# Kernel tuning notes

Measured on AMD Instinct MI355X. Metric: run time of the kernel, lower is better.

Reference implementation:

```python
import jax, jax.numpy as jnp
import numpy as np

L = 512       # seq_len (capped by hard-coded max_length=512)
LEN = 2048    # input feature dim ('length')
D = 2048      # d_model
H = 16        # num_heads
DH = D // H   # d_head = 128
FF = 8192     # FFN hidden
EPS = 1e-5


def _pos_encoding(n, d):
    # Matches PositionalEncoderLayer buffer construction exactly.
    pos = jnp.arange(n, dtype=jnp.float32)[:, None]                              # [n,1]
    freqs = 1.0 / (2.0 * jnp.pi) / (10000.0 * jnp.exp(jnp.arange(0, d, 2, dtype=jnp.float32) / d))
    pe = jnp.zeros((n, d), dtype=jnp.float32)
    pe = pe.at[:, 0::2].set(jnp.sin(2.0 * jnp.pi * freqs * pos))
    pe = pe.at[:, 1::2].set(jnp.cos(2.0 * jnp.pi * freqs * pos))
    return pe


def _layernorm(x, g, b):
    mu = jnp.mean(x, axis=-1, keepdims=True)
    var = jnp.mean((x - mu) ** 2, axis=-1, keepdims=True)
    return (x - mu) / jnp.sqrt(var + EPS) * g + b


def setup_inputs() -> dict:
    key = jax.random.key(0)
    ks = jax.random.split(key, 12)
    def lin(k, fin, fout):
        kw, kb = jax.random.split(k)
        W = jax.random.normal(kw, (fin, fout), jnp.float32) / np.sqrt(fin)
        b = jax.random.normal(kb, (fout,), jnp.float32) * 0.01
        return W, b
    emb_W, emb_b = lin(ks[0], LEN, D)
    Wq, bq = lin(ks[1], D, D)
    Wk, bk = lin(ks[2], D, D)
    Wv, bv = lin(ks[3], D, D)
    Wo, bo = lin(ks[4], D, D)
    W1, b1 = lin(ks[5], D, FF)
    W2, b2 = lin(ks[6], FF, D)
    return {
        "sequence": jax.random.normal(ks[7], (L, LEN), jnp.float32),
        "emb_W": emb_W, "emb_b": emb_b,
        "Wq": Wq, "bq": bq, "Wk": Wk, "bk": bk, "Wv": Wv, "bv": bv,
        "Wo": Wo, "bo": bo,
        "ln_g": jnp.ones((D,), jnp.float32), "ln_b": jnp.zeros((D,), jnp.float32),
        "W1": W1, "b1": b1, "W2": W2, "b2": b2,
    }


def reference(sequence, emb_W, emb_b, Wq, bq, Wk, bk, Wv, bv, Wo, bo, ln_g, ln_b, W1, b1, W2, b2):
    # Embedding + positional encoding
    X = sequence @ emb_W + emb_b                         # [L, D]
    X = X + _pos_encoding(X.shape[0], X.shape[1])
    # Multi-head attention (keeps the module's [L, d_head, H] layout)
    Q = (X @ Wq + bq).reshape(-1, DH, H)
    K = (X @ Wk + bk).reshape(-1, DH, H)
    V = (X @ Wv + bv).reshape(-1, DH, H)
    scores = jnp.einsum('ldh,mdh->lmh', Q, K) / jnp.sqrt(jnp.float32(D))  # [L, L, H]
    attn = jax.nn.softmax(scores, axis=1)                # softmax over keys
    A = jnp.einsum('lmh,mdh->ldh', attn, V).reshape(-1, D) @ Wo + bo
    # Residual + shared LayerNorm, FFN, residual + shared LayerNorm
    Xa = _layernorm(A + X, ln_g, ln_b)
    F = jax.nn.gelu(Xa @ W1 + b1) @ W2 + b2
    return _layernorm(F + Xa, ln_g, ln_b)
```

## Files before the change

kernel.cpp:

```cpp
#include <hip/hip_runtime.h>
#include <hip/hip_bf16.h>


typedef __bf16 bf16_t;
typedef __bf16 bf16x4 __attribute__((ext_vector_type(4)));
typedef __bf16 bf16x8 __attribute__((ext_vector_type(8)));
typedef float  f32x4  __attribute__((ext_vector_type(4)));

#define SEQL 512
#define DM   2048
#define FFH  8192
#define NH   16
#define DHD  128
#define PST  ((size_t)SEQL*DM)

__device__ __forceinline__ unsigned short bfbits(float f){
  bf16_t h = (bf16_t)f;
  return __builtin_bit_cast(unsigned short, h);
}
__device__ __forceinline__ unsigned int pack2(float a, float b){
  return (unsigned int)bfbits(a) | ((unsigned int)bfbits(b) << 16);
}

__device__ __forceinline__ void gll16(const bf16_t* g, bf16_t* l){
  __builtin_amdgcn_global_load_lds(
      (const __attribute__((address_space(1))) void*)g,
      (__attribute__((address_space(3))) void*)l, 16, 0, 0);
}
__device__ __forceinline__ unsigned lds_off(const void* p){
  return (unsigned)(uintptr_t)(const __attribute__((address_space(3))) void*)p;
}

struct CvtSeg { const float* src; bf16_t* dst; int base; };
struct CvtA4  { CvtSeg s[4]; };

template<int NS>
__device__ __forceinline__ void cvt_block8k(const CvtSeg* segs, int b){
  int i = 0;
#pragma unroll
  for (int j = 1; j < NS; ++j) if (b >= segs[j].base) i = j;
  const float* src = segs[i].src;
  bf16_t* dst = segs[i].dst;
  const size_t off0 = (size_t)(b - segs[i].base) * 8192 + threadIdx.x * 8;
  f32x4 v[8];
#pragma unroll
  for (int it = 0; it < 4; ++it){
    v[2*it]   = *(const f32x4*)(src + off0 + it*2048);
    v[2*it+1] = *(const f32x4*)(src + off0 + it*2048 + 4);
  }
#pragma unroll
  for (int it = 0; it < 4; ++it){
    uint4 o;
    o.x = pack2(v[2*it][0],   v[2*it][1]);
    o.y = pack2(v[2*it][2],   v[2*it][3]);
    o.z = pack2(v[2*it+1][0], v[2*it+1][1]);
    o.w = pack2(v[2*it+1][2], v[2*it+1][3]);
    *(uint4*)(dst + off0 + it*2048) = o;
  }
}

template<int NS>
__global__ __launch_bounds__(256)
void cvt8k(CvtA4 a){ cvt_block8k<NS>(a.s, blockIdx.x); }

constexpr int E_PART = 0;
constexpr int E_QKV  = 1;
constexpr int E_FFN1 = 2;

template<int EPI, int PERM, int BM, int NCVT>
__global__ __launch_bounds__(256, (BM == 64) ? 3 : 4)
void gemmT(const bf16_t* __restrict__ A,
           const bf16_t* __restrict__ B0, const bf16_t* __restrict__ B1,
           const bf16_t* __restrict__ B2,
           const float* __restrict__ b0p, const float* __restrict__ b1p,
           const float* __restrict__ b2p,
           float* __restrict__ outF, bf16_t* __restrict__ o0,
           bf16_t* __restrict__ o1, bf16_t* __restrict__ o2,
           int nn, int Nw, int K, int Kc, int gemmN, CvtA4 cva)
{
  if constexpr (NCVT > 0){
    if ((int)blockIdx.x >= gemmN){
      cvt_block8k<NCVT>(cva.s, (int)blockIdx.x - gemmN);
      return;
    }
  }
  constexpr int NF    = (BM == 64) ? 4 : 2;
  constexpr int APASS = BM / 32;
  constexpr int MTM   = (BM == 64) ? 7 : 15;
  constexpr int MTS   = (BM == 64) ? 3 : 4;
  __shared__ bf16_t sA[2][BM*64];
  __shared__ bf16_t sB[2][128*64];
  const int tid  = threadIdx.x;
  const int lane = tid & 63, w = tid >> 6;
  const int wr4 = (BM == 64) ? (w >> 1) : 0;
  const int wc  = (BM == 64) ? (w & 1)  : w;
  const int c = lane & 15, g = lane >> 4;

  const int cpx = gemmN >> 3;
  const int sblk = ((int)blockIdx.x & 7) * cpx + ((int)blockIdx.x >> 3);
  const int mt = sblk & MTM, q2 = sblk >> MTS;
  const int nt = q2 % nn, zt = q2 / nn;
  const int m0 = mt * BM, k0 = zt * Kc;

  const bf16_t* Bsel = B0; int nb0 = nt * 128;
  if constexpr (EPI == E_QKV){
    if (nt >= 32){ Bsel = B2; nb0 = (nt - 32) * 128; }
    else if (nt >= 16){ Bsel = B1; nb0 = (nt - 16) * 128; }
  }

  const int arow = tid >> 3;
  const int acol = (((tid & 7) ^ ((tid >> 3) & 7)) << 3);
  const bf16_t* Aps[APASS];
#pragma unroll
  for (int pa = 0; pa < APASS; ++pa)
    Aps[pa] = A + (size_t)(m0 + pa*32 + arow) * K + k0 + acol;

  const int klB  = (lane >> 3) * 4 + ((lane >> 1) & 3);
  const int colB = nb0 + w*16 + (lane & 1)*8;
  const bf16_t* Bph[2];
  if constexpr (!PERM){
#pragma unroll
    for (int h = 0; h < 2; ++h)
      Bph[h] = Bsel + (size_t)(k0 + h*32 + klB) * Nw + colB;
  }

  const unsigned sBbase[2] = { lds_off(&sB[0][0]), lds_off(&sB[1][0]) };
  const unsigned trLane = (unsigned)(g*256 + c*8);

  f32x4 acc[2][NF] = {};
  const int nk = Kc >> 6;

#define STAGE(bf, kt) {                                                     \
    _Pragma("unroll")                                                       \
    for (int pa = 0; pa < APASS; ++pa)                                      \
      gll16(Aps[pa] + (size_t)(kt)*64, &sA[bf][(pa*256 + tid)*8]);          \
    _Pragma("unroll")                                                       \
    for (int h = 0; h < 2; ++h)                                             \
      _Pragma("unroll")                                                     \
      for (int p = 0; p < 2; ++p){                                          \
        const bf16_t* src;                                                  \
        if constexpr (PERM){                                                \
          const int kr = k0 + (kt)*64 + h*32 + klB;                         \
          const int krow = ((kr & 127) << 4) + (kr >> 7);                   \
          src = Bsel + (size_t)krow * Nw + colB + p*64;                     \
        } else {                                                            \
          src = Bph[h] + (size_t)(kt)*64*Nw + p*64;                         \
        }                                                                   \
        gll16(src, &sB[bf][h*4096 + (p*256 + tid)*8]);                      \
      } }

#define COMPUTE(PB) {                                                       \
    bf16x8 af[2][2]; bf16x8 bq[NF][2];                                      \
    _Pragma("unroll")                                                       \
    for (int m = 0; m < 2; ++m)                                             \
      _Pragma("unroll")                                                     \
      for (int ks = 0; ks < 2; ++ks){                                       \
        const int r = wr4*32 + m*16 + c;                                    \
        af[m][ks] = *(const bf16x8*)&sA[PB][r*64 + (((ks*4+g) ^ (r&7))<<3)];\
      }                                                                     \
    { const unsigned base = sBbase[PB] + (unsigned)(wc*NF*1024) + trLane;   \
      _Pragma("unroll")                                                     \
      for (int n = 0; n < NF; ++n)                                          \
        _Pragma("unroll")                                                   \
        for (int ks = 0; ks < 2; ++ks){                                     \
          bf16x4 r0, r1;                                                    \
          const unsigned a2 = base + (unsigned)(n*1024 + ks*8192);          \
          asm volatile("ds_read_b64_tr_b16 %0, %1" : "=v"(r0) : "v"(a2));   \
          asm volatile("ds_read_b64_tr_b16 %0, %1 offset:128" : "=v"(r1) : "v"(a2)); \
          bq[n][ks] = __builtin_shufflevector(r0, r1, 0,1,2,3,4,5,6,7);     \
        } }                                                                 \
    asm volatile("s_waitcnt lgkmcnt(0)" ::: "memory");                      \
    __builtin_amdgcn_sched_barrier(0);                                      \
    _Pragma("unroll")                                                       \
    for (int m = 0; m < 2; ++m)                                             \
      _Pragma("unroll")                                                     \
      for (int n = 0; n < NF; ++n)                                          \
        _Pragma("unroll")                                                   \
        for (int ks = 0; ks < 2; ++ks)                                      \
          acc[m][n] = __builtin_amdgcn_mfma_f32_16x16x32_bf16(af[m][ks], bq[n][ks], acc[m][n], 0,0,0); }

#define WAIT_NL() {                                                         \
    if constexpr (BM == 64) asm volatile("s_waitcnt vmcnt(6)" ::: "memory");\
    else                    asm volatile("s_waitcnt vmcnt(5)" ::: "memory");}

  STAGE(0, 0);
  STAGE(1, 1);
  WAIT_NL();
  __builtin_amdgcn_s_barrier();
  __builtin_amdgcn_sched_barrier(0);

  int buf = 0;
  for (int kt = 0; kt < nk; ++kt){
    COMPUTE(buf);
    __builtin_amdgcn_s_barrier();
    __builtin_amdgcn_sched_barrier(0);
    if (kt + 1 < nk){
      if (kt + 2 < nk){
        STAGE(buf, kt + 2);
        WAIT_NL();
      } else {
        asm volatile("s_waitcnt vmcnt(0)" ::: "memory");
      }
      __builtin_amdgcn_s_barrier();
      __builtin_amdgcn_sched_barrier(0);
    }
    buf ^= 1;
  }
#undef STAGE
#undef COMPUTE
#undef WAIT_NL

#pragma unroll
  for (int n = 0; n < NF; ++n){
    const int col = nt*128 + wc*(NF*16) + n*16 + c;
#pragma unroll
    for (int m = 0; m < 2; ++m){
      const int row0 = m0 + wr4*32 + m*16 + 4*g;
      const f32x4 a4 = acc[m][n];
      if constexpr (EPI == E_PART){
        float* dst = outF + (size_t)zt * PST;
#pragma unroll
        for (int rr = 0; rr < 4; ++rr)
          dst[(size_t)(row0+rr)*DM + col] = a4[rr];
      } else if constexpr (EPI == E_QKV){
        if (col < DM){
          const float bv = b0p[col];
#pragma unroll
          for (int rr = 0; rr < 4; ++rr)
            o0[(size_t)(row0+rr)*DM + col] = (bf16_t)(a4[rr] + bv);
        } else if (col < 2*DM){
          const int cc = col - DM;
          const float bv = b1p[cc];
#pragma unroll
          for (int rr = 0; rr < 4; ++rr)
            o1[(size_t)(row0+rr)*DM + cc] = (bf16_t)(a4[rr] + bv);
        } else {
          const int cc = col - 2*DM;
          const float bv = b2p[cc];
          const int hh = cc & 15, dd = cc >> 4;
          unsigned short us[4];
#pragma unroll
          for (int rr = 0; rr < 4; ++rr) us[rr] = bfbits(a4[rr] + bv);
          *(ushort4*)&o2[(size_t)(hh*DHD + dd)*SEQL + row0] =
              make_ushort4(us[0], us[1], us[2], us[3]);
        }
      } else if constexpr (EPI == E_FFN1){
        const float bv = b0p[col];
#pragma unroll
        for (int rr = 0; rr < 4; ++rr){
          const float v = a4[rr] + bv;
          const float z = v * (v*v*0.044715f + 1.0f) * 1.5957691216f;
          const float gg = v / (1.0f + __expf(-z));
          o0[(size_t)(row0+rr)*FFH + col] = (bf16_t)gg;
        }
      }
    }
  }
}

__global__ __launch_bounds__(256)
void permute_qk(const bf16_t* __restrict__ Qf, const bf16_t* __restrict__ Kf,
                bf16_t* __restrict__ Qhd, bf16_t* __restrict__ Khd)
{
  const int row = blockIdx.x, which = blockIdx.y, tid = threadIdx.x;
  const bf16_t* src = (which ? Kf : Qf) + (size_t)row * DM;
  bf16_t* dst = which ? Khd : Qhd;
  const int hh = tid >> 4, d0 = (tid & 15) * 8;
  unsigned short us[8];
#pragma unroll
  for (int j = 0; j < 8; ++j)
    us[j] = __builtin_bit_cast(unsigned short, src[(d0 + j)*NH + hh]);
  uint4 o;
  o.x = (unsigned)us[0] | ((unsigned)us[1] << 16);
  o.y = (unsigned)us[2] | ((unsigned)us[3] << 16);
  o.z = (unsigned)us[4] | ((unsigned)us[5] << 16);
  o.w = (unsigned)us[6] | ((unsigned)us[7] << 16);
  *(uint4*)&dst[(size_t)hh*(SEQL*DHD) + (size_t)row*DHD + d0] = o;
}

template<int NCVT>
__global__ __launch_bounds__(256)
void attn_cvt(const bf16_t* __restrict__ Qh, const bf16_t* __restrict__ Kh,
              const bf16_t* __restrict__ Vt, bf16_t* __restrict__ Aout,
              int attnN, CvtA4 cva)
{
  if constexpr (NCVT > 0){
    if ((int)blockIdx.x >= attnN){
      cvt_block8k<NCVT>(cva.s, (int)blockIdx.x - attnN);
      return;
    }
  }
  __shared__ bf16_t Pl[32*512];
  __shared__ float redm[4][32];
  __shared__ float reds[4][32];
  const int tid = threadIdx.x;
  const int lane = tid & 63, w = tid >> 6;
  const int c = lane & 15, g = lane >> 4;
  const int h  = (int)blockIdx.x >> 4;
  const int rb = ((int)blockIdx.x & 15) * 32;
  const bf16_t* Qb = Qh + (size_t)h * (SEQL*DHD);
  const bf16_t* Kb = Kh + (size_t)h * (SEQL*DHD);
  const bf16_t* Vb = Vt + (size_t)h * (SEQL*DHD);

  bf16x8 qf[2][4];
#pragma unroll
  for (int a = 0; a < 2; ++a)
#pragma unroll
    for (int ks = 0; ks < 4; ++ks)
      qf[a][ks] = *(const bf16x8*)(Qb + (size_t)(rb + a*16 + c)*DHD + ks*32 + g*8);

  f32x4 s[2][8] = {};
#pragma unroll
  for (int ks = 0; ks < 4; ++ks)
#pragma unroll
    for (int b = 0; b < 8; ++b){
      const bf16x8 kf = *(const bf16x8*)(Kb + (size_t)(w*128 + b*16 + c)*DHD + ks*32 + g*8);
      s[0][b] = __builtin_amdgcn_mfma_f32_16x16x32_bf16(qf[0][ks], kf, s[0][b], 0,0,0);
      s[1][b] = __builtin_amdgcn_mfma_f32_16x16x32_bf16(qf[1][ks], kf, s[1][b], 0,0,0);
    }
#pragma unroll
  for (int a = 0; a < 2; ++a)
#pragma unroll
    for (int b = 0; b < 8; ++b)
#pragma unroll
      for (int rr = 0; rr < 4; ++rr) s[a][b][rr] *= 0.022097086912079612f;

  float mx[2][4], sm[2][4], inv[2][4];
#pragma unroll
  for (int a = 0; a < 2; ++a)
#pragma unroll
    for (int rr = 0; rr < 4; ++rr){
      float m = s[a][0][rr];
#pragma unroll
      for (int b = 1; b < 8; ++b) m = fmaxf(m, s[a][b][rr]);
#pragma unroll
      for (int off = 1; off < 16; off <<= 1) m = fmaxf(m, __shfl_xor(m, off));
      mx[a][rr] = m;
    }
  if (c == 0)
#pragma unroll
    for (int a = 0; a < 2; ++a)
#pragma unroll
      for (int rr = 0; rr < 4; ++rr) redm[w][a*16 + 4*g + rr] = mx[a][rr];
  __syncthreads();
#pragma unroll
  for (int a = 0; a < 2; ++a)
#pragma unroll
    for (int rr = 0; rr < 4; ++rr){
      const int lr = a*16 + 4*g + rr;
      mx[a][rr] = fmaxf(fmaxf(redm[0][lr], redm[1][lr]), fmaxf(redm[2][lr], redm[3][lr]));
      sm[a][rr] = 0.f;
    }
#pragma unroll
  for (int a = 0; a < 2; ++a)
#pragma unroll
    for (int b = 0; b < 8; ++b)
#pragma unroll
      for (int rr = 0; rr < 4; ++rr){
        const float p = __expf(s[a][b][rr] - mx[a][rr]);
        s[a][b][rr] = p;
        sm[a][rr] += p;
      }
#pragma unroll
  for (int a = 0; a < 2; ++a)
#pragma unroll
    for (int rr = 0; rr < 4; ++rr){
#pragma unroll
      for (int off = 1; off < 16; off <<= 1) sm[a][rr] += __shfl_xor(sm[a][rr], off);
    }
  if (c == 0)
#pragma unroll
    for (int a = 0; a < 2; ++a)
#pragma unroll
      for (int rr = 0; rr < 4; ++rr) reds[w][a*16 + 4*g + rr] = sm[a][rr];
  __syncthreads();
#pragma unroll
  for (int a = 0; a < 2; ++a)
#pragma unroll
    for (int rr = 0; rr < 4; ++rr){
      const int lr = a*16 + 4*g + rr;
      inv[a][rr] = 1.0f / (reds[0][lr] + reds[1][lr] + reds[2][lr] + reds[3][lr]);
    }

#pragma unroll
  for (int a = 0; a < 2; ++a)
#pragma unroll
    for (int b = 0; b < 8; ++b)
#pragma unroll
      for (int rr = 0; rr < 4; ++rr){
        const int lr  = a*16 + 4*g + rr;
        const int key = w*128 + b*16 + c;
        const int slot = (key >> 3) ^ (lr & 7);
        Pl[lr*512 + slot*8 + (key & 7)] = (bf16_t)(s[a][b][rr] * inv[a][rr]);
      }
  __syncthreads();

  f32x4 o[2][2] = {};
  const int dw = w * 32;
#pragma unroll
  for (int kst = 0; kst < 16; ++kst){
    bf16x8 pa2[2];
#pragma unroll
    for (int a = 0; a < 2; ++a){
      const int r = a*16 + c;
      const int slot = (kst*4 + g) ^ (r & 7);
      pa2[a] = *(const bf16x8*)&Pl[r*512 + slot*8];
    }
#pragma unroll
    for (int db = 0; db < 2; ++db){
      const bf16x8 vf = *(const bf16x8*)(Vb + (size_t)(dw + db*16 + c)*SEQL + kst*32 + g*8);
      o[0][db] = __builtin_amdgcn_mfma_f32_16x16x32_bf16(pa2[0], vf, o[0][db], 0,0,0);
      o[1][db] = __builtin_amdgcn_mfma_f32_16x16x32_bf16(pa2[1], vf, o[1][db], 0,0,0);
    }
  }
#pragma unroll
  for (int a = 0; a < 2; ++a)
#pragma unroll
    for (int db = 0; db < 2; ++db)
#pragma unroll
      for (int rr = 0; rr < 4; ++rr){
        const int row  = rb + a*16 + 4*g + rr;
        const int col2 = h*DHD + dw + db*16 + c;
        Aout[(size_t)row*DM + col2] = (bf16_t)o[a][db][rr];
      }
}

template<int S>
__global__ __launch_bounds__(256)
void reduce_pos(const float* __restrict__ P, const float* __restrict__ bias,
                float* __restrict__ X, bf16_t* __restrict__ XB)
{
  const int row = blockIdx.x, c0 = threadIdx.x * 8;
  const size_t base = (size_t)row * DM + c0;
  float y[8];
#pragma unroll
  for (int j = 0; j < 8; ++j) y[j] = bias[c0 + j];
#pragma unroll
  for (int s = 0; s < S; ++s){
    const float4 v0 = *(const float4*)(P + s*PST + base);
    const float4 v1 = *(const float4*)(P + s*PST + base + 4);
    y[0]+=v0.x; y[1]+=v0.y; y[2]+=v0.z; y[3]+=v0.w;
    y[4]+=v1.x; y[5]+=v1.y; y[6]+=v1.z; y[7]+=v1.w;
  }
#pragma unroll
  for (int j = 0; j < 8; ++j){
    const int col = c0 + j;
    const float fr  = 1e-4f * __expf(-(float)(col >> 1) * (1.0f/1024.0f));
    const float ang = (float)row * fr;
    y[j] += (col & 1) ? __cosf(ang) : __sinf(ang);
  }
  *(float4*)(X + base)     = make_float4(y[0], y[1], y[2], y[3]);
  *(float4*)(X + base + 4) = make_float4(y[4], y[5], y[6], y[7]);
  uint4 ob;
  ob.x = pack2(y[0], y[1]); ob.y = pack2(y[2], y[3]);
  ob.z = pack2(y[4], y[5]); ob.w = pack2(y[6], y[7]);
  *(uint4*)&XB[base] = ob;
}

template<int S, int WB>
__global__ __launch_bounds__(256)
void reduce_ln(const float* __restrict__ P, const float* __restrict__ bias,
               const float* __restrict__ resid, const float* __restrict__ gam,
               const float* __restrict__ bet, float* __restrict__ outF,
               bf16_t* __restrict__ outB)
{
  const int row = blockIdx.x, tid = threadIdx.x, c0 = tid * 8;
  const size_t base = (size_t)row * DM + c0;
  float y[8];
  {
    const float4 r0 = *(const float4*)(resid + base);
    const float4 r1 = *(const float4*)(resid + base + 4);
    y[0]=r0.x; y[1]=r0.y; y[2]=r0.z; y[3]=r0.w;
    y[4]=r1.x; y[5]=r1.y; y[6]=r1.z; y[7]=r1.w;
  }
#pragma unroll
  for (int j = 0; j < 8; ++j) y[j] += bias[c0 + j];
#pragma unroll
  for (int s = 0; s < S; ++s){
    const float4 v0 = *(const float4*)(P + s*PST + base);
    const float4 v1 = *(const float4*)(P + s*PST + base + 4);
    y[0]+=v0.x; y[1]+=v0.y; y[2]+=v0.z; y[3]+=v0.w;
    y[4]+=v1.x; y[5]+=v1.y; y[6]+=v1.z; y[7]+=v1.w;
  }
  float sm = 0.f, qs = 0.f;
#pragma unroll
  for (int j = 0; j < 8; ++j){ sm += y[j]; qs += y[j]*y[j]; }
#pragma unroll
  for (int off = 32; off >= 1; off >>= 1){
    sm += __shfl_xor(sm, off); qs += __shfl_xor(qs, off);
  }
  __shared__ float rs[4], rq[4];
  const int w = tid >> 6;
  if ((tid & 63) == 0){ rs[w] = sm; rq[w] = qs; }
  __syncthreads();
  sm = rs[0]+rs[1]+rs[2]+rs[3];
  qs = rq[0]+rq[1]+rq[2]+rq[3];
  const float mu   = sm * (1.0f/2048.0f);
  const float var  = qs * (1.0f/2048.0f) - mu*mu;
  const float rstd = rsqrtf(var + 1e-5f);
  const float4 g0 = *(const float4*)(gam + c0);
  const float4 g1 = *(const float4*)(gam + c0 + 4);
  const float4 b0 = *(const float4*)(bet + c0);
  const float4 b1 = *(const float4*)(bet + c0 + 4);
  float o[8];
  o[0] = (y[0]-mu)*rstd*g0.x + b0.x;  o[1] = (y[1]-mu)*rstd*g0.y + b0.y;
  o[2] = (y[2]-mu)*rstd*g0.z + b0.z;  o[3] = (y[3]-mu)*rstd*g0.w + b0.w;
  o[4] = (y[4]-mu)*rstd*g1.x + b1.x;  o[5] = (y[5]-mu)*rstd*g1.y + b1.y;
  o[6] = (y[6]-mu)*rstd*g1.z + b1.z;  o[7] = (y[7]-mu)*rstd*g1.w + b1.w;
  *(float4*)(outF + base)     = make_float4(o[0], o[1], o[2], o[3]);
  *(float4*)(outF + base + 4) = make_float4(o[4], o[5], o[6], o[7]);
  if constexpr (WB){
    uint4 ob;
    ob.x = pack2(o[0], o[1]); ob.y = pack2(o[2], o[3]);
    ob.z = pack2(o[4], o[5]); ob.w = pack2(o[6], o[7]);
    *(uint4*)&outB[base] = ob;
  }
}

extern "C" void kernel_launch(void* const* d_in, const int* in_sizes, int n_in,
                              void* d_out, int out_size, void* d_ws, size_t ws_size,
                              hipStream_t stream)
{
  const float* seq   = (const float*)d_in[0];
  const float* emb_W = (const float*)d_in[1];
  const float* emb_b = (const float*)d_in[2];
  const float* Wq = (const float*)d_in[3];  const float* bq = (const float*)d_in[4];
  const float* Wk = (const float*)d_in[5];  const float* bk = (const float*)d_in[6];
  const float* Wv = (const float*)d_in[7];  const float* bv = (const float*)d_in[8];
  const float* Wo = (const float*)d_in[9];  const float* bo = (const float*)d_in[10];
  const float* ln_g = (const float*)d_in[11]; const float* ln_b = (const float*)d_in[12];
  const float* W1 = (const float*)d_in[13]; const float* b1 = (const float*)d_in[14];
  const float* W2 = (const float*)d_in[15]; const float* b2 = (const float*)d_in[16];

  char* ws = (char*)d_ws;
  size_t off = 0;
  auto take = [&](size_t bytes) -> void* {
    void* p = ws + off;
    off += (bytes + 255) & ~(size_t)255;
    return p;
  };
  bf16_t* seqB = (bf16_t*)take((size_t)SEQL*DM*2);
  bf16_t* WeB  = (bf16_t*)take((size_t)DM*DM*2);
  bf16_t* WqB  = (bf16_t*)take((size_t)DM*DM*2);
  bf16_t* WkB  = (bf16_t*)take((size_t)DM*DM*2);
  bf16_t* WvB  = (bf16_t*)take((size_t)DM*DM*2);
  bf16_t* WoB  = (bf16_t*)take((size_t)DM*DM*2);
  bf16_t* W1B  = (bf16_t*)take((size_t)DM*FFH*2);
  bf16_t* W2B  = (bf16_t*)take((size_t)FFH*DM*2);
  float*  X    = (float*) take((size_t)SEQL*DM*4);
  bf16_t* XB   = (bf16_t*)take((size_t)SEQL*DM*2);
  bf16_t* Qf   = (bf16_t*)take((size_t)SEQL*DM*2);
  bf16_t* Kf   = (bf16_t*)take((size_t)SEQL*DM*2);
  bf16_t* Qhd  = (bf16_t*)take((size_t)SEQL*DM*2);
  bf16_t* Khd  = (bf16_t*)take((size_t)SEQL*DM*2);
  bf16_t* Vt   = (bf16_t*)take((size_t)SEQL*DM*2);
  bf16_t* Afl  = (bf16_t*)take((size_t)SEQL*DM*2);
  float*  Pp   = (float*) take((size_t)8*SEQL*DM*4);
  float*  Xa   = (float*) take((size_t)SEQL*DM*4);
  bf16_t* XaB  = (bf16_t*)take((size_t)SEQL*DM*2);
  bf16_t* Hb   = (bf16_t*)take((size_t)SEQL*FFH*2);
  (void)ws_size; (void)in_sizes; (void)n_in; (void)out_size;

  CvtA4 cz = {};

  CvtA4 c0 = {};
  c0.s[0] = { seq,   seqB, 0 };
  c0.s[1] = { emb_W, WeB,  128 };
  cvt8k<2><<<dim3(640), 256, 0, stream>>>(c0);

  CvtA4 cq = {};
  cq.s[0] = { Wq, WqB, 0 };
  cq.s[1] = { Wk, WkB, 512 };
  cq.s[2] = { Wv, WvB, 1024 };
  cq.s[3] = { Wo, WoB, 1536 };
  gemmT<E_PART,0,64,4><<<dim3(2560), 256, 0, stream>>>(seqB, WeB, nullptr, nullptr,
      nullptr, nullptr, nullptr, Pp, nullptr, nullptr, nullptr, 16, DM, DM, 512, 512, cq);
  reduce_pos<4><<<SEQL, 256, 0, stream>>>(Pp, emb_b, X, XB);

  CvtA4 c1 = {};
  c1.s[0] = { W1, W1B, 0 };
  gemmT<E_QKV,0,32,1><<<dim3(2816), 256, 0, stream>>>(XB, WqB, WkB, WvB,
      bq, bk, bv, nullptr, Qf, Kf, Vt, 48, DM, DM, DM, 768, c1);
  permute_qk<<<dim3(SEQL,2), 256, 0, stream>>>(Qf, Kf, Qhd, Khd);

  CvtA4 c2 = {};
  c2.s[0] = { W2, W2B, 0 };
  attn_cvt<1><<<dim3(2304), 256, 0, stream>>>(Qhd, Khd, Vt, Afl, 256, c2);

  gemmT<E_PART,1,64,0><<<dim3(512), 256, 0, stream>>>(Afl, WoB, nullptr, nullptr,
      nullptr, nullptr, nullptr, Pp, nullptr, nullptr, nullptr, 16, DM, DM, 512, 512, cz);
  reduce_ln<4,1><<<SEQL, 256, 0, stream>>>(Pp, bo, X, ln_g, ln_b, Xa, XaB);

  gemmT<E_FFN1,0,32,0><<<dim3(1024), 256, 0, stream>>>(XaB, W1B, nullptr, nullptr,
      b1, nullptr, nullptr, nullptr, Hb, nullptr, nullptr, 64, FFH, DM, DM, 1024, cz);

  gemmT<E_PART,0,64,0><<<dim3(1024), 256, 0, stream>>>(Hb, W2B, nullptr, nullptr,
      nullptr, nullptr, nullptr, Pp, nullptr, nullptr, nullptr, 16, DM, FFH, 1024, 1024, cz);
  reduce_ln<8,0><<<SEQL, 256, 0, stream>>>(Pp, b2, Xa, ln_g, ln_b, (float*)d_out, nullptr);
}
```

Baseline: 222.6 us.

## Stream weight conversion with fewer persistent double-buffered blocks; halve FFN2 split-K

The fp32-to-bf16 conversion helpers now use a grid-strided loop. Each block processes several 8K-element chunks, double-buffering the loads of the next chunk against the stores of the current one. This replaces many one-shot blocks, so the fused GEMM and attention launches carry far fewer trailing conversion blocks. Separately, the FFN2 GEMM goes from 8 to 4 K-splits, halving partial-sum traffic and the reduce work, at the cost of less parallelism per block.

```diff
diff --git a/kernel.cpp b/kernel.cpp
--- a/kernel.cpp
+++ b/kernel.cpp
@@ -31,37 +31,53 @@
   return (unsigned)(uintptr_t)(const __attribute__((address_space(3))) void*)p;
 }
 
-struct CvtSeg { const float* src; bf16_t* dst; int base; };
+struct CvtSeg { const float* src; bf16_t* dst; int base; int nblk; int iters; };
 struct CvtA4  { CvtSeg s[4]; };
 
 template<int NS>
-__device__ __forceinline__ void cvt_block8k(const CvtSeg* segs, int b){
+__device__ __forceinline__ void cvt_stream(const CvtSeg* segs, int b){
   int i = 0;
 #pragma unroll
   for (int j = 1; j < NS; ++j) if (b >= segs[j].base) i = j;
-  const float* src = segs[i].src;
-  bf16_t* dst = segs[i].dst;
-  const size_t off0 = (size_t)(b - segs[i].base) * 8192 + threadIdx.x * 8;
-  f32x4 v[8];
-#pragma unroll
-  for (int it = 0; it < 4; ++it){
-    v[2*it]   = *(const f32x4*)(src + off0 + it*2048);
-    v[2*it+1] = *(const f32x4*)(src + off0 + it*2048 + 4);
-  }
-#pragma unroll
-  for (int it = 0; it < 4; ++it){
-    uint4 o;
-    o.x = pack2(v[2*it][0],   v[2*it][1]);
-    o.y = pack2(v[2*it][2],   v[2*it][3]);
-    o.z = pack2(v[2*it+1][0], v[2*it+1][1]);
-    o.w = pack2(v[2*it+1][2], v[2*it+1][3]);
-    *(uint4*)(dst + off0 + it*2048) = o;
-  }
+  const float* __restrict__ src = segs[i].src;
+  bf16_t* __restrict__ dst = segs[i].dst;
+  const int rb = b - segs[i].base;
+  const int iters = segs[i].iters;
+  const size_t step = (size_t)segs[i].nblk * 8192;
+  size_t off = (size_t)rb * 8192 + threadIdx.x * 8;
+
+  f32x4 va[8], vb[8];
+#define CLOAD(V, o) { _Pragma("unroll")                                     \
+    for (int s2 = 0; s2 < 4; ++s2){                                         \
+      V[2*s2]   = *(const f32x4*)(src + (o) + s2*2048);                     \
+      V[2*s2+1] = *(const f32x4*)(src + (o) + s2*2048 + 4); } }
+#define CSTORE(V, o) { _Pragma("unroll")                                    \
+    for (int s2 = 0; s2 < 4; ++s2){                                         \
+      uint4 u;                                                              \
+      u.x = pack2(V[2*s2][0],   V[2*s2][1]);                                \
+      u.y = pack2(V[2*s2][2],   V[2*s2][3]);                                \
+      u.z = pack2(V[2*s2+1][0], V[2*s2+1][1]);                              \
+      u.w = pack2(V[2*s2+1][2], V[2*s2+1][3]);                              \
+      *(uint4*)(dst + (o) + s2*2048) = u; } }
+
+  CLOAD(va, off);
+  for (int it = 0; it < iters; ++it){
+    const size_t cur = off;
+    off += step;
+    if (it + 1 < iters){
+      if (it & 1){ CLOAD(va, off); CSTORE(vb, cur); }
+      else       { CLOAD(vb, off); CSTORE(va, cur); }
+    } else {
+      if (it & 1){ CSTORE(vb, cur); } else { CSTORE(va, cur); }
+    }
+  }
+#undef CLOAD
+#undef CSTORE
 }
 
 template<int NS>
 __global__ __launch_bounds__(256)
-void cvt8k(CvtA4 a){ cvt_block8k<NS>(a.s, blockIdx.x); }
+void cvt8k(CvtA4 a){ cvt_stream<NS>(a.s, blockIdx.x); }
 
 constexpr int E_PART = 0;
 constexpr int E_QKV  = 1;
@@ -80,7 +96,7 @@
 {
   if constexpr (NCVT > 0){
     if ((int)blockIdx.x >= gemmN){
-      cvt_block8k<NCVT>(cva.s, (int)blockIdx.x - gemmN);
+      cvt_stream<NCVT>(cva.s, (int)blockIdx.x - gemmN);
       return;
     }
   }
@@ -286,7 +302,7 @@
 {
   if constexpr (NCVT > 0){
     if ((int)blockIdx.x >= attnN){
-      cvt_block8k<NCVT>(cva.s, (int)blockIdx.x - attnN);
+      cvt_stream<NCVT>(cva.s, (int)blockIdx.x - attnN);
       return;
     }
   }
@@ -564,28 +580,28 @@
   CvtA4 cz = {};
 
   CvtA4 c0 = {};
-  c0.s[0] = { seq,   seqB, 0 };
-  c0.s[1] = { emb_W, WeB,  128 };
-  cvt8k<2><<<dim3(640), 256, 0, stream>>>(c0);
+  c0.s[0] = { seq,   seqB,  0, 32,  4 };
+  c0.s[1] = { emb_W, WeB,  32, 128, 4 };
+  cvt8k<2><<<dim3(160), 256, 0, stream>>>(c0);
 
   CvtA4 cq = {};
-  cq.s[0] = { Wq, WqB, 0 };
-  cq.s[1] = { Wk, WkB, 512 };
-  cq.s[2] = { Wv, WvB, 1024 };
-  cq.s[3] = { Wo, WoB, 1536 };
-  gemmT<E_PART,0,64,4><<<dim3(2560), 256, 0, stream>>>(seqB, WeB, nullptr, nullptr,
+  cq.s[0] = { Wq, WqB,   0, 128, 4 };
+  cq.s[1] = { Wk, WkB, 128, 128, 4 };
+  cq.s[2] = { Wv, WvB, 256, 128, 4 };
+  cq.s[3] = { Wo, WoB, 384, 128, 4 };
+  gemmT<E_PART,0,64,4><<<dim3(1024), 256, 0, stream>>>(seqB, WeB, nullptr, nullptr,
       nullptr, nullptr, nullptr, Pp, nullptr, nullptr, nullptr, 16, DM, DM, 512, 512, cq);
   reduce_pos<4><<<SEQL, 256, 0, stream>>>(Pp, emb_b, X, XB);
 
   CvtA4 c1 = {};
-  c1.s[0] = { W1, W1B, 0 };
-  gemmT<E_QKV,0,32,1><<<dim3(2816), 256, 0, stream>>>(XB, WqB, WkB, WvB,
+  c1.s[0] = { W1, W1B, 0, 256, 8 };
+  gemmT<E_QKV,0,32,1><<<dim3(1024), 256, 0, stream>>>(XB, WqB, WkB, WvB,
       bq, bk, bv, nullptr, Qf, Kf, Vt, 48, DM, DM, DM, 768, c1);
   permute_qk<<<dim3(SEQL,2), 256, 0, stream>>>(Qf, Kf, Qhd, Khd);
 
   CvtA4 c2 = {};
-  c2.s[0] = { W2, W2B, 0 };
-  attn_cvt<1><<<dim3(2304), 256, 0, stream>>>(Qhd, Khd, Vt, Afl, 256, c2);
+  c2.s[0] = { W2, W2B, 0, 256, 8 };
+  attn_cvt<1><<<dim3(512), 256, 0, stream>>>(Qhd, Khd, Vt, Afl, 256, c2);
 
   gemmT<E_PART,1,64,0><<<dim3(512), 256, 0, stream>>>(Afl, WoB, nullptr, nullptr,
       nullptr, nullptr, nullptr, Pp, nullptr, nullptr, nullptr, 16, DM, DM, 512, 512, cz);
@@ -594,7 +610,7 @@
   gemmT<E_FFN1,0,32,0><<<dim3(1024), 256, 0, stream>>>(XaB, W1B, nullptr, nullptr,
       b1, nullptr, nullptr, nullptr, Hb, nullptr, nullptr, 64, FFH, DM, DM, 1024, cz);
 
-  gemmT<E_PART,0,64,0><<<dim3(1024), 256, 0, stream>>>(Hb, W2B, nullptr, nullptr,
-      nullptr, nullptr, nullptr, Pp, nullptr, nullptr, nullptr, 16, DM, FFH, 1024, 1024, cz);
-  reduce_ln<8,0><<<SEQL, 256, 0, stream>>>(Pp, b2, Xa, ln_g, ln_b, (float*)d_out, nullptr);
-}
+  gemmT<E_PART,0,64,0><<<dim3(512), 256, 0, stream>>>(Hb, W2B, nullptr, nullptr,
+      nullptr, nullptr, nullptr, Pp, nullptr, nullptr, nullptr, 16, DM, FFH, 2048, 512, cz);
+  reduce_ln<4,0><<<SEQL, 256, 0, stream>>>(Pp, b2, Xa, ln_g, ln_b, (float*)d_out, nullptr);
+}
```

New measurement: 224.8 us. No clear change (+1.0%).
